# Kernel tuning notes

Hardware: AMD Instinct MI355X
Metric: run time of the kernel (lower is better)

## Reference

```python
import jax, jax.numpy as jnp
import numpy as np

H, B, S, E, V, C = 1024, 1024, 128, 6, 3, 10


def setup_inputs() -> dict:
    key = jax.random.key(0)
    ks = jax.random.split(key, 18)
    sH = 1.0 / np.sqrt(H)

    def n(k, shape, scale):
        return (jax.random.normal(k, shape, dtype=jnp.float32) * scale)

    return {
        'x': jax.random.randint(ks[0], (B, S), 0, V),
        'emb': n(ks[1], (V, E), 1.0),
        'W_gx': n(ks[2], (H, E), 1.0 / np.sqrt(E)),
        'W_gh': n(ks[3], (H, H), sH),
        'b_g': n(ks[4], (H, 1), sH),
        'W_ix': n(ks[5], (H, E), 1.0 / np.sqrt(E)),
        'W_ih': n(ks[6], (H, H), sH),
        'b_i': n(ks[7], (H, 1), sH),
        'W_fx': n(ks[8], (H, E), 1.0 / np.sqrt(E)),
        'W_fh': n(ks[9], (H, H), sH),
        'b_f': n(ks[10], (H, 1), sH),
        'W_ox': n(ks[11], (H, E), 1.0 / np.sqrt(E)),
        'W_oh': n(ks[12], (H, H), sH),
        'b_o': n(ks[13], (H, 1), sH),
        'W_ph': n(ks[14], (C, H), sH),
        'b_p': n(ks[15], (C, 1), sH),
        'h_init': n(ks[16], (H, B), 1.0),
        'c_init': n(ks[17], (H, B), 1.0),
    }


def reference(x, emb, W_gx, W_gh, b_g, W_ix, W_ih, b_i, W_fx, W_fh, b_f,
              W_ox, W_oh, b_o, W_ph, b_p, h_init, c_init):
    T = x.shape[1] - 1  # torch loop runs over seq_length - 1 steps
    e = emb[x[:, :T]]  # [B, T, E]
    # Precompute all input-to-gate projections in one batched contraction each.
    Xg = jnp.einsum('he,bte->thb', W_gx, e)  # [T, H, B]
    Xi = jnp.einsum('he,bte->thb', W_ix, e)
    Xf = jnp.einsum('he,bte->thb', W_fx, e)
    Xo = jnp.einsum('he,bte->thb', W_ox, e)

    def step(carry, xs):
        h, c = carry  # [H, B]
        xg, xi, xf, xo = xs
        g = jnp.tanh(xg + W_gh @ h + b_g)
        i = jax.nn.sigmoid(xi + W_ih @ h + b_i)
        f = jax.nn.sigmoid(xf + W_fh @ h + b_f)
        o = jax.nn.sigmoid(xo + W_oh @ h + b_o)
        c2 = g * i + c * f
        h2 = jnp.tanh(c2) * o
        return (h2, c2), None

    (h, c), _ = jax.lax.scan(step, (h_init, c_init), (Xg, Xi, Xf, Xo))
    p = W_ph @ h + b_p  # [C, B]
    return jax.nn.log_softmax(p.T, axis=-1)  # [B, C]
```

## Files before the change

### kernel.cpp

```cpp
#include <hip/hip_runtime.h>

constexpr int kH = 1024;
constexpr int kB = 1024;
constexpr int kS = 128;
constexpr int kT = 127;
constexpr int kE = 6;
constexpr int kV = 3;
constexpr int kC = 10;

typedef short s16x8 __attribute__((ext_vector_type(8)));
typedef short s16x4 __attribute__((ext_vector_type(4)));
typedef float f32x4 __attribute__((ext_vector_type(4)));
typedef int   i32x2 __attribute__((ext_vector_type(2)));
typedef int   i32x4 __attribute__((ext_vector_type(4)));
typedef unsigned short u16;

__device__ __forceinline__ float b2f(u16 u) {
    return __uint_as_float(((unsigned)u) << 16);
}
__device__ __forceinline__ u16 f2b(float f) {
    unsigned u = __float_as_uint(f);
    return (u16)((u + 0x7FFFu + ((u >> 16) & 1u)) >> 16);
}
__device__ __forceinline__ float sigmoid_fast(float x) {
    return 1.0f / (1.0f + __expf(-x));
}
__device__ __forceinline__ float tanh_fast(float x) {
    return 2.0f / (1.0f + __expf(-2.0f * x)) - 1.0f;
}
__device__ __forceinline__ float clamp30(float x) {
    return fminf(fmaxf(x, -30.0f), 30.0f);
}

__device__ __forceinline__ void async_copy16(const u16* g, u16* l) {
    __builtin_amdgcn_global_load_lds(
        (const __attribute__((address_space(1))) void*)g,
        (__attribute__((address_space(3))) void*)l, 16, 0, 0);
}

__global__ __launch_bounds__(256) void prep_weights(
    const float* __restrict__ Wgh, const float* __restrict__ Wih,
    const float* __restrict__ Wfh, const float* __restrict__ Woh,
    u16* __restrict__ wsw)
{
    unsigned grp = blockIdx.x * 256 + threadIdx.x;
    const int lane = grp & 63;
    const int lm   = lane & 15;
    const int quad = lane >> 4;
    const int k0   = (grp >> 6) & 7;
    const int g    = (grp >> 9) & 3;
    const int kc   = (grp >> 11) & 3;
    const int by   = grp >> 13;
    const float* src = (g == 0) ? Wgh : (g == 1) ? Wih : (g == 2) ? Wfh : Woh;
    const int row = by * 16 + lm;
    const int k   = kc * 256 + k0 * 32 + quad * 8;
    f32x4 v0 = *(const f32x4*)(src + (size_t)row * kH + k);
    f32x4 v1 = *(const f32x4*)(src + (size_t)row * kH + k + 4);
    s16x8 o;
#pragma unroll
    for (int j = 0; j < 4; ++j) o[j] = (short)f2b(v0[j]);
#pragma unroll
    for (int j = 0; j < 4; ++j) o[4 + j] = (short)f2b(v1[j]);
    *(s16x8*)(wsw + (size_t)grp * 8) = o;
}

__global__ __launch_bounds__(1024) void prep_hc(
    const float* __restrict__ h0, const float* __restrict__ c0,
    u16* __restrict__ hA, float* __restrict__ cT)
{
    __shared__ float th[32][33];
    __shared__ float tc[32][33];
    int b = blockIdx.x * 32 + threadIdx.x;
    int h = blockIdx.y * 32 + threadIdx.y;
    th[threadIdx.y][threadIdx.x] = h0[(size_t)h * kB + b];
    tc[threadIdx.y][threadIdx.x] = c0[(size_t)h * kB + b];
    __syncthreads();
    int ob = blockIdx.x * 32 + threadIdx.y;
    int oh = blockIdx.y * 32 + threadIdx.x;
    hA[(size_t)ob * kH + oh] = f2b(th[threadIdx.x][threadIdx.y]);
    cT[(size_t)ob * kH + oh] = tc[threadIdx.x][threadIdx.y];
}

__global__ __launch_bounds__(256) void prep_q(
    const float* __restrict__ Wgx, const float* __restrict__ Wix,
    const float* __restrict__ Wfx, const float* __restrict__ Wox,
    const float* __restrict__ bg,  const float* __restrict__ bi,
    const float* __restrict__ bf_, const float* __restrict__ bo,
    const float* __restrict__ emb, float* __restrict__ Qp,
    int* __restrict__ flags)
{
    int tid = blockIdx.x * blockDim.x + threadIdx.x;
    if (tid < 512) flags[tid] = 0;
    if (tid >= 4096) return;
    int g   = tid >> 10;
    int hr4 = (tid & 1023) >> 2;
    int v   = tid & 3;
    const float* Wx = (g == 0) ? Wgx : (g == 1) ? Wix : (g == 2) ? Wfx : Wox;
    const float* bb = (g == 0) ? bg  : (g == 1) ? bi  : (g == 2) ? bf_ : bo;
    f32x4 o;
#pragma unroll
    for (int reg = 0; reg < 4; ++reg) {
        int row = hr4 * 4 + reg;
        float s = bb[row];
        if (v < kV) {
#pragma unroll
            for (int e = 0; e < kE; ++e) s += Wx[row * kE + e] * emb[v * kE + e];
        }
        o[reg] = s;
    }
    *(f32x4*)(Qp + (size_t)tid * 4) = o;
}

__global__ __launch_bounds__(512, 2) void lstm_persist(
    const u16* __restrict__ wsw, const float* __restrict__ Qp,
    const int* __restrict__ x,
    short* __restrict__ hA, short* __restrict__ hB,
    const float* __restrict__ cT, int* __restrict__ flags)
{
    __shared__ u16 wlds[65536];

    const int tid  = threadIdx.x;
    const int lane = tid & 63;
    const int wave = tid >> 6;
    const int lm   = lane & 15;
    const int quad = lane >> 4;
    const int blk  = blockIdx.x;
    const int xcd  = blk & 7;
    const int slot = blk >> 3;
    const int by   = xcd * 8 + (slot & 7);
    const int bx   = slot >> 3;
    const int r0 = by * 16;
    const int c0 = bx * 256 + wave * 32;

    const u16* wswblk = wsw + (size_t)by * 65536;

#pragma unroll
    for (int rr = 0; rr < 16; ++rr) {
        const int ub = wave * 8192 + rr * 512;
        async_copy16(wswblk + ub + lane * 8, &wlds[ub]);
    }

    f32x4 creg[2];
#pragma unroll
    for (int nt = 0; nt < 2; ++nt)
        creg[nt] = *(const f32x4*)(cT +
            (size_t)(c0 + nt * 16 + lm) * kH + r0 + quad * 4);

    const int* xp0 = x + (size_t)(c0 + lm) * kS;
    const int* xp1 = x + (size_t)(c0 + 16 + lm) * kS;
    const int koff = quad * 8;

    asm volatile("s_waitcnt vmcnt(0)" ::: "memory");
    __syncthreads();

#pragma unroll 1
    for (int t = 0; t < kT; ++t) {
        const short* hin  = (t & 1) ? hB : hA;
        short*       hout = (t & 1) ? hA : hB;

        int vv[2];
        {
            int v0 = xp0[t]; vv[0] = (v0 < 0) ? 0 : (v0 > kV - 1) ? (kV - 1) : v0;
            int v1 = xp1[t]; vv[1] = (v1 < 0) ? 0 : (v1 > kV - 1) ? (kV - 1) : v1;
        }
        f32x4 qv[2][4];
#pragma unroll
        for (int nt = 0; nt < 2; ++nt)
#pragma unroll
            for (int g = 0; g < 4; ++g)
                qv[nt][g] = *(const f32x4*)(Qp +
                    (size_t)(((g * 256 + by * 4 + quad) * 4 + vv[nt]) * 4));

        const short* hrow0 = hin + (size_t)(c0 + lm) * kH + koff;
        const short* hrow1 = hin + (size_t)(c0 + 16 + lm) * kH + koff;
        s16x8 br[6][2];
#pragma unroll
        for (int s = 0; s < 5; ++s) {
            br[s][0] = *(const s16x8*)(hrow0 + s * 32);
            br[s][1] = *(const s16x8*)(hrow1 + s * 32);
        }

        f32x4 acc[4][2];
        const f32x4 zero = {0.f, 0.f, 0.f, 0.f};
#pragma unroll
        for (int g = 0; g < 4; ++g)
#pragma unroll
            for (int n = 0; n < 2; ++n) acc[g][n] = zero;

#pragma unroll
        for (int k0 = 0; k0 < 32; ++k0) {
            if (k0 + 5 < 32) {
                const int s = (k0 + 5) % 6;
                br[s][0] = *(const s16x8*)(hrow0 + (k0 + 5) * 32);
                br[s][1] = *(const s16x8*)(hrow1 + (k0 + 5) * 32);
            }
            const int cur = k0 % 6;
            const int cb = (k0 >> 3) * 16384;
#pragma unroll
            for (int g = 0; g < 4; ++g) {
                const int f = cb + ((g * 8 + (k0 & 7)) * 64 + lane) * 8;
                s16x8 a = *(const s16x8*)&wlds[f];
                acc[g][0] = __builtin_amdgcn_mfma_f32_16x16x32_bf16(a, br[cur][0], acc[g][0], 0, 0, 0);
                acc[g][1] = __builtin_amdgcn_mfma_f32_16x16x32_bf16(a, br[cur][1], acc[g][1], 0, 0, 0);
            }
        }

#pragma unroll
        for (int nt = 0; nt < 2; ++nt) {
            const int c = c0 + nt * 16 + lm;
            const int rb = r0 + quad * 4;
            f32x4 cnew;
            s16x4 hnew;
#pragma unroll
            for (int reg = 0; reg < 4; ++reg) {
                float pg = clamp30(acc[0][nt][reg] + qv[nt][0][reg]);
                float pi = clamp30(acc[1][nt][reg] + qv[nt][1][reg]);
                float pf = clamp30(acc[2][nt][reg] + qv[nt][2][reg]);
                float po = clamp30(acc[3][nt][reg] + qv[nt][3][reg]);
                float gg = tanh_fast(pg);
                float ii = sigmoid_fast(pi);
                float ff = sigmoid_fast(pf);
                float oo = sigmoid_fast(po);
                float c2 = gg * ii + creg[nt][reg] * ff;
                c2 = fminf(fmaxf(c2, -200.0f), 200.0f);
                cnew[reg] = c2;
                hnew[reg] = (short)f2b(tanh_fast(c2) * oo);
            }
            creg[nt] = cnew;
            i32x2 hv;
            __builtin_memcpy(&hv, &hnew, 8);
            short* hp = hout + (size_t)c * kH + rb;
            asm volatile("global_store_dwordx2 %0, %1, off sc0 sc1"
                         :: "v"(hp), "v"(hv) : "memory");
        }

        if (t < kT - 1) {
            asm volatile("s_waitcnt vmcnt(0)" ::: "memory");
            __syncthreads();
            if (tid < 64) {
                if (tid == 0) {
                    int* fp = flags + blk;
                    int fv = t + 1;
                    asm volatile("global_store_dword %0, %1, off sc0 sc1\n\t"
                                 "s_waitcnt vmcnt(0)"
                                 :: "v"(fp), "v"(fv) : "memory");
                }
                const int* fp = flags + lane * 4;
                for (;;) {
                    i32x4 fa;
                    asm volatile(
                        "global_load_dwordx4 %0, %1, off sc0 sc1\n\t"
                        "s_waitcnt vmcnt(0)"
                        : "=&v"(fa) : "v"(fp) : "memory");
                    int ok = (fa.x > t) & (fa.y > t) & (fa.z > t) & (fa.w > t);
                    if (__all(ok)) break;
                    __builtin_amdgcn_s_sleep(1);
                }
                __builtin_amdgcn_fence(__ATOMIC_ACQUIRE, "agent");
            }
            __syncthreads();
        }
    }
}

__global__ __launch_bounds__(256) void logits_kernel(
    const u16* __restrict__ hT, const float* __restrict__ Wph,
    const float* __restrict__ bp, float* __restrict__ out)
{
    const int wave = threadIdx.x >> 6;
    const int lane = threadIdx.x & 63;
    const int b = blockIdx.x * 4 + wave;

    const u16* hp = hT + (size_t)b * kH + lane * 16;
    float hf[16];
#pragma unroll
    for (int j = 0; j < 16; ++j) hf[j] = b2f(hp[j]);

    float p[kC];
#pragma unroll
    for (int cls = 0; cls < kC; ++cls) {
        const float* wp = Wph + (size_t)cls * kH + lane * 16;
        float s = 0.f;
#pragma unroll
        for (int j = 0; j < 16; ++j) s += hf[j] * wp[j];
#pragma unroll
        for (int off = 1; off < 64; off <<= 1) s += __shfl_xor(s, off, 64);
        p[cls] = fminf(fmaxf(s + bp[cls], -1.0e4f), 1.0e4f);
    }

    float m = p[0];
#pragma unroll
    for (int cls = 1; cls < kC; ++cls) m = fmaxf(m, p[cls]);
    float se = 0.f;
#pragma unroll
    for (int cls = 0; cls < kC; ++cls) se += __expf(p[cls] - m);
    float l = m + __logf(se);

    if (lane < kC) {
        float myp = p[0];
#pragma unroll
        for (int cls = 1; cls < kC; ++cls)
            if (lane == cls) myp = p[cls];
        out[(size_t)b * kC + lane] = myp - l;
    }
}

extern "C" void kernel_launch(void* const* d_in, const int* in_sizes, int n_in,
                              void* d_out, int out_size, void* d_ws, size_t ws_size,
                              hipStream_t stream)
{
    const int*   x   = (const int*)  d_in[0];
    const float* emb = (const float*)d_in[1];
    const float* Wgx = (const float*)d_in[2];
    const float* Wgh = (const float*)d_in[3];
    const float* bg  = (const float*)d_in[4];
    const float* Wix = (const float*)d_in[5];
    const float* Wih = (const float*)d_in[6];
    const float* bi  = (const float*)d_in[7];
    const float* Wfx = (const float*)d_in[8];
    const float* Wfh = (const float*)d_in[9];
    const float* bf_ = (const float*)d_in[10];
    const float* Wox = (const float*)d_in[11];
    const float* Woh = (const float*)d_in[12];
    const float* bo  = (const float*)d_in[13];
    const float* Wph = (const float*)d_in[14];
    const float* bp  = (const float*)d_in[15];
    const float* h0  = (const float*)d_in[16];
    const float* c0  = (const float*)d_in[17];

    char* ws = (char*)d_ws;
    float* Qp  = (float*)ws;
    u16*   hA  = (u16*)(ws + (64 << 10));
    u16*   hB  = hA + (size_t)kB * kH;
    float* cT  = (float*)(hB + (size_t)kB * kH);
    u16*   wsw = (u16*)(cT + (size_t)kB * kH);
    int*   flags = (int*)(wsw + (size_t)64 * 65536);

    prep_weights<<<dim3(2048), dim3(256), 0, stream>>>(Wgh, Wih, Wfh, Woh, wsw);
    prep_hc<<<dim3(kB / 32, kH / 32), dim3(32, 32), 0, stream>>>(h0, c0, hA, cT);
    prep_q<<<dim3(16), dim3(256), 0, stream>>>(Wgx, Wix, Wfx, Wox, bg, bi, bf_, bo,
                                               emb, Qp, flags);

    lstm_persist<<<dim3(256), dim3(512), 0, stream>>>(
        wsw, Qp, x, (short*)hA, (short*)hB, cT, flags);

    logits_kernel<<<dim3(kB / 4), dim3(256), 0, stream>>>(hB, Wph, bp, (float*)d_out);
}
```

Before: 2.760 ms.

## Localize per-step barrier to batch groups mapped by hardware XCC id

Each block reads its XCC id from a hardware register and takes an atomic rank, so the blocks sharing a batch slice sit on the same pair of XCDs. The per-timestep barrier now only waits for the 64 blocks that produce that slice's h, instead of all 256 blocks. One leader per XCC polls the group flags and publishes a release word, which the other blocks on that XCC poll before invalidating their cache. The h-operand prefetch depth also doubles to 10 slices, and those loads are issued before the gate-input loads. This relies on exactly 32 blocks landing on each XCC; if that does not hold, the mapping breaks or deadlocks.

```diff
diff --git a/kernel.cpp b/kernel.cpp
--- a/kernel.cpp
+++ b/kernel.cpp
@@ -12,7 +12,6 @@
 typedef short s16x4 __attribute__((ext_vector_type(4)));
 typedef float f32x4 __attribute__((ext_vector_type(4)));
 typedef int   i32x2 __attribute__((ext_vector_type(2)));
-typedef int   i32x4 __attribute__((ext_vector_type(4)));
 typedef unsigned short u16;
 
 __device__ __forceinline__ float b2f(u16 u) {
@@ -87,10 +86,10 @@
     const float* __restrict__ bg,  const float* __restrict__ bi,
     const float* __restrict__ bf_, const float* __restrict__ bo,
     const float* __restrict__ emb, float* __restrict__ Qp,
-    int* __restrict__ flags)
+    int* __restrict__ ctrl)
 {
     int tid = blockIdx.x * blockDim.x + threadIdx.x;
-    if (tid < 512) flags[tid] = 0;
+    if (tid < 512) ctrl[tid] = 0;
     if (tid >= 4096) return;
     int g   = tid >> 10;
     int hr4 = (tid & 1023) >> 2;
@@ -115,24 +114,37 @@
     const u16* __restrict__ wsw, const float* __restrict__ Qp,
     const int* __restrict__ x,
     short* __restrict__ hA, short* __restrict__ hB,
-    const float* __restrict__ cT, int* __restrict__ flags)
+    const float* __restrict__ cT, int* __restrict__ ctrl)
 {
     __shared__ u16 wlds[65536];
+    __shared__ int sh_ids[2];
 
     const int tid  = threadIdx.x;
     const int lane = tid & 63;
     const int wave = tid >> 6;
     const int lm   = lane & 15;
     const int quad = lane >> 4;
-    const int blk  = blockIdx.x;
-    const int xcd  = blk & 7;
-    const int slot = blk >> 3;
-    const int by   = xcd * 8 + (slot & 7);
-    const int bx   = slot >> 3;
-    const int r0 = by * 16;
-    const int c0 = bx * 256 + wave * 32;
-
-    const u16* wswblk = wsw + (size_t)by * 65536;
+
+    if (tid == 0) {
+        unsigned xccr;
+        asm volatile("s_getreg_b32 %0, hwreg(HW_REG_XCC_ID)" : "=s"(xccr));
+        int rank = atomicAdd(ctrl + 264 + (xccr & 7), 1);
+        sh_ids[0] = (int)(xccr & 7);
+        sh_ids[1] = rank;
+    }
+    __syncthreads();
+    const int xcc  = sh_ids[0];
+    const int rank = sh_ids[1];
+    const int p    = xcc >> 1;
+    const int q    = (xcc & 1) * 32 + rank;
+    const bool leader = (rank == 0);
+    const int r0 = q * 16;
+    const int c0 = p * 256 + wave * 32;
+
+    int* flags   = ctrl;
+    int* release = ctrl + 256;
+
+    const u16* wswblk = wsw + (size_t)q * 65536;
 
 #pragma unroll
     for (int rr = 0; rr < 16; ++rr) {
@@ -158,6 +170,15 @@
         const short* hin  = (t & 1) ? hB : hA;
         short*       hout = (t & 1) ? hA : hB;
 
+        const short* hrow0 = hin + (size_t)(c0 + lm) * kH + koff;
+        const short* hrow1 = hin + (size_t)(c0 + 16 + lm) * kH + koff;
+        s16x8 br[12][2];
+#pragma unroll
+        for (int s = 0; s < 10; ++s) {
+            br[s][0] = *(const s16x8*)(hrow0 + s * 32);
+            br[s][1] = *(const s16x8*)(hrow1 + s * 32);
+        }
+
         int vv[2];
         {
             int v0 = xp0[t]; vv[0] = (v0 < 0) ? 0 : (v0 > kV - 1) ? (kV - 1) : v0;
@@ -169,16 +190,7 @@
 #pragma unroll
             for (int g = 0; g < 4; ++g)
                 qv[nt][g] = *(const f32x4*)(Qp +
-                    (size_t)(((g * 256 + by * 4 + quad) * 4 + vv[nt]) * 4));
-
-        const short* hrow0 = hin + (size_t)(c0 + lm) * kH + koff;
-        const short* hrow1 = hin + (size_t)(c0 + 16 + lm) * kH + koff;
-        s16x8 br[6][2];
-#pragma unroll
-        for (int s = 0; s < 5; ++s) {
-            br[s][0] = *(const s16x8*)(hrow0 + s * 32);
-            br[s][1] = *(const s16x8*)(hrow1 + s * 32);
-        }
+                    (size_t)(((g * 256 + q * 4 + quad) * 4 + vv[nt]) * 4));
 
         f32x4 acc[4][2];
         const f32x4 zero = {0.f, 0.f, 0.f, 0.f};
@@ -189,12 +201,12 @@
 
 #pragma unroll
         for (int k0 = 0; k0 < 32; ++k0) {
-            if (k0 + 5 < 32) {
-                const int s = (k0 + 5) % 6;
-                br[s][0] = *(const s16x8*)(hrow0 + (k0 + 5) * 32);
-                br[s][1] = *(const s16x8*)(hrow1 + (k0 + 5) * 32);
-            }
-            const int cur = k0 % 6;
+            if (k0 + 10 < 32) {
+                const int s = (k0 + 10) % 12;
+                br[s][0] = *(const s16x8*)(hrow0 + (k0 + 10) * 32);
+                br[s][1] = *(const s16x8*)(hrow1 + (k0 + 10) * 32);
+            }
+            const int cur = k0 % 12;
             const int cb = (k0 >> 3) * 16384;
 #pragma unroll
             for (int g = 0; g < 4; ++g) {
@@ -237,26 +249,46 @@
         if (t < kT - 1) {
             asm volatile("s_waitcnt vmcnt(0)" ::: "memory");
             __syncthreads();
-            if (tid < 64) {
-                if (tid == 0) {
-                    int* fp = flags + blk;
-                    int fv = t + 1;
+            if (tid == 0) {
+                int* fp = flags + p * 64 + q;
+                int fv = t + 1;
+                asm volatile("global_store_dword %0, %1, off sc0 sc1\n\t"
+                             "s_waitcnt vmcnt(0)"
+                             :: "v"(fp), "v"(fv) : "memory");
+            }
+            if (leader && tid < 64) {
+                const int* fp = flags + p * 64 + lane;
+                for (;;) {
+                    int fvv;
+                    asm volatile(
+                        "global_load_dword %0, %1, off sc0 sc1\n\t"
+                        "s_waitcnt vmcnt(0)"
+                        : "=v"(fvv) : "v"(fp) : "memory");
+                    if (__all(fvv > t)) break;
+                    __builtin_amdgcn_s_sleep(1);
+                }
+                if (lane == 0) {
+                    asm volatile("buffer_inv sc1\n\t"
+                                 "s_waitcnt vmcnt(0)" ::: "memory");
+                    int* rp = release + xcc;
+                    int rv = t + 1;
                     asm volatile("global_store_dword %0, %1, off sc0 sc1\n\t"
                                  "s_waitcnt vmcnt(0)"
-                                 :: "v"(fp), "v"(fv) : "memory");
+                                 :: "v"(rp), "v"(rv) : "memory");
                 }
-                const int* fp = flags + lane * 4;
+            }
+            if (tid < 64) {
+                const int* rp = release + xcc;
                 for (;;) {
-                    i32x4 fa;
+                    int rvv;
                     asm volatile(
-                        "global_load_dwordx4 %0, %1, off sc0 sc1\n\t"
+                        "global_load_dword %0, %1, off sc0 sc1\n\t"
                         "s_waitcnt vmcnt(0)"
-                        : "=&v"(fa) : "v"(fp) : "memory");
-                    int ok = (fa.x > t) & (fa.y > t) & (fa.z > t) & (fa.w > t);
-                    if (__all(ok)) break;
+                        : "=v"(rvv) : "v"(rp) : "memory");
+                    if (__all(rvv > t)) break;
                     __builtin_amdgcn_s_sleep(1);
                 }
-                __builtin_amdgcn_fence(__ATOMIC_ACQUIRE, "agent");
+                asm volatile("buffer_inv" ::: "memory");
             }
             __syncthreads();
         }
@@ -334,15 +366,15 @@
     u16*   hB  = hA + (size_t)kB * kH;
     float* cT  = (float*)(hB + (size_t)kB * kH);
     u16*   wsw = (u16*)(cT + (size_t)kB * kH);
-    int*   flags = (int*)(wsw + (size_t)64 * 65536);
+    int*   ctrl = (int*)(wsw + (size_t)64 * 65536);
 
     prep_weights<<<dim3(2048), dim3(256), 0, stream>>>(Wgh, Wih, Wfh, Woh, wsw);
     prep_hc<<<dim3(kB / 32, kH / 32), dim3(32, 32), 0, stream>>>(h0, c0, hA, cT);
     prep_q<<<dim3(16), dim3(256), 0, stream>>>(Wgx, Wix, Wfx, Wox, bg, bi, bf_, bo,
-                                               emb, Qp, flags);
+                                               emb, Qp, ctrl);
 
     lstm_persist<<<dim3(256), dim3(512), 0, stream>>>(
-        wsw, Qp, x, (short*)hA, (short*)hB, cT, flags);
+        wsw, Qp, x, (short*)hA, (short*)hB, cT, ctrl);
 
     logits_kernel<<<dim3(kB / 4), dim3(256), 0, stream>>>(hB, Wph, bp, (float*)d_out);
 }
```

Result: faster. 2.523 ms (-8.6%).
